# Optimization experiments

Hardware: AMD Instinct MI355X
Metric: run time of the kernel (lower is better)

Reference implementation:

```python
import jax, jax.numpy as jnp
import numpy as np

B, D, DC, K = 65536, 768, 192, 100  # batch patterns, hidden_dim, codebook_hidden, num_clusters
LN_EPS = 1e-5


def setup_inputs() -> dict:
    key = jax.random.key(0)
    ks = jax.random.split(key, 12)
    w = lambda k, shape: (jax.random.normal(k, shape, jnp.float32) * 0.02)
    return {
        "hidden": jax.random.normal(ks[0], (B, D), jnp.float32),
        "W_low": w(ks[1], (DC, D)),   # nn.Linear(hidden_dim, codebook_hidden), torch (out,in)
        "b_low": jnp.zeros((DC,), jnp.float32),
        "ln_g": jnp.ones((DC,), jnp.float32),
        "ln_b": jnp.zeros((DC,), jnp.float32),
        "Wq": w(ks[2], (DC, DC)),
        "Wk": w(ks[3], (DC, DC)),
        "Wv": w(ks[4], (DC, DC)),
        "Wo": w(ks[5], (DC, DC)),
        "codebook": w(ks[6], (K, DC)),  # vp_codebook.weight
        "W_high": w(ks[7], (D, DC)),    # nn.Linear(codebook_hidden, hidden_dim)
        "b_high": jnp.zeros((D,), jnp.float32),
    }


def reference(hidden, W_low, b_low, ln_g, ln_b, Wq, Wk, Wv, Wo, codebook, W_high, b_high):
    # low projection: 768 -> 192
    pat = hidden @ W_low.T + b_low  # [B, DC]
    # LayerNorm over last dim
    mu = jnp.mean(pat, axis=-1, keepdims=True)
    var = jnp.mean(jnp.square(pat - mu), axis=-1, keepdims=True)
    pat = (pat - mu) * jax.lax.rsqrt(var + LN_EPS) * ln_g + ln_b
    # CrossAttention against codebook with NEGATED scores (distance-like)
    q = pat @ Wq.T            # [B, DC]
    k = codebook @ Wk.T       # [K, DC]
    v = codebook @ Wv.T       # [K, DC]
    scores = -(q @ k.T)       # [B, K]
    attn_w = jax.nn.softmax(scores, axis=-1)
    attn_out = (attn_w @ v) @ Wo.T  # [B, DC]
    # argmin over attention weights -> codebook selection + gather
    idx = jnp.argmin(attn_w, axis=-1)   # [B] int
    z_q = codebook[idx]                 # [B, DC]
    # high projection on both branches
    pat_h = attn_out @ W_high.T + b_high  # [B, D]
    zq_h = z_q @ W_high.T + b_high        # [B, D]
    # straight-through estimator: pat + (z_q - pat).detach()
    return pat_h + jax.lax.stop_gradient(zq_h - pat_h)
```

## Files before the change

### kernel.cpp

```cpp
#include <hip/hip_runtime.h>

#define NB    65536
#define DIN   768
#define DCB   192
#define KCL   100
#define NJ    112
#define RT    128
#define KC    64

#define OFF_KTIL 0
#define OFF_S    19200
#define OFF_CS   38400
#define OFF_U    38512
#define OFF_T    38624
#define OFF_MT   38736
#define OFF_ZH   124752
#define OFF_FLAG 201552


__global__ void kA1(const float* __restrict__ cb, const float* __restrict__ Wk,
                    float* __restrict__ ktil, int* __restrict__ flag) {
  __shared__ float cbrow[DCB];
  int j = blockIdx.x, i = threadIdx.x;
  if (j == 0 && i == 0) *flag = 0;
  cbrow[i] = cb[j*DCB + i];
  __syncthreads();
  const float4* wr = (const float4*)&Wk[(size_t)i * DCB];
  double s0 = 0.0, s1 = 0.0;
  #pragma unroll 4
  for (int m4 = 0; m4 < DCB/4; m4++) {
    float4 w = wr[m4];
    s0 += (double)w.x * (double)cbrow[m4*4+0] + (double)w.z * (double)cbrow[m4*4+2];
    s1 += (double)w.y * (double)cbrow[m4*4+1] + (double)w.w * (double)cbrow[m4*4+3];
  }
  ktil[j*DCB+i] = (float)(s0 + s1);
}

__global__ void kA2(const float* __restrict__ Wq, const float* __restrict__ ktil,
                    const float* __restrict__ ln_g, const float* __restrict__ ln_b,
                    const float* __restrict__ b_low,
                    float* __restrict__ S, float* __restrict__ csum,
                    float* __restrict__ tv, float* __restrict__ u,
                    int* __restrict__ flag) {
  __shared__ float krow[DCB];
  __shared__ double red[DCB];
  int j = blockIdx.x, c = threadIdx.x;
  krow[c] = ktil[j*DCB + c];
  __syncthreads();
  double a0 = 0.0, a1 = 0.0;
  #pragma unroll 4
  for (int i = 0; i < DCB; i += 2) {
    a0 += (double)Wq[i*DCB+c]     * (double)krow[i];
    a1 += (double)Wq[(i+1)*DCB+c] * (double)krow[i+1];
  }
  double a = a0 + a1;
  float Sv = ln_g[c] * (float)a;
  S[j*DCB+c] = Sv;

  red[c] = (double)Sv; __syncthreads();
  if (c == 0) {
    double p0=0,p1=0,p2=0,p3=0;
    for (int i = 0; i < DCB; i += 4) { p0+=red[i]; p1+=red[i+1]; p2+=red[i+2]; p3+=red[i+3]; }
    csum[j] = (float)(p0+p1+p2+p3);
  }
  __syncthreads();
  red[c] = (double)ln_b[c] * a; __syncthreads();
  if (c == 0) {
    double p0=0,p1=0,p2=0,p3=0;
    for (int i = 0; i < DCB; i += 4) { p0+=red[i]; p1+=red[i+1]; p2+=red[i+2]; p3+=red[i+3]; }
    float tf = (float)(p0+p1+p2+p3); tv[j] = tf;
    if (tf != 0.0f) atomicOr(flag, 1);
  }
  __syncthreads();
  red[c] = (double)b_low[c] * (double)Sv; __syncthreads();
  if (c == 0) {
    double p0=0,p1=0,p2=0,p3=0;
    for (int i = 0; i < DCB; i += 4) { p0+=red[i]; p1+=red[i+1]; p2+=red[i+2]; p3+=red[i+3]; }
    u[j] = (float)(p0+p1+p2+p3);
  }
  __syncthreads();
  if (j == 0) {
    red[c] = (double)b_low[c]; __syncthreads();
    if (c == 0) {
      double p0=0,p1=0,p2=0,p3=0;
      for (int i = 0; i < DCB; i += 4) { p0+=red[i]; p1+=red[i+1]; p2+=red[i+2]; p3+=red[i+3]; }
      u[KCL] = (float)((p0+p1+p2+p3) / (double)DCB);
      for (int p = KCL+1; p < NJ; p++) u[p] = 0.f;
      for (int p = KCL;   p < NJ; p++) { csum[p] = 0.f; tv[p] = 0.f; }
    }
  }
}

__global__ void kA3(const float* __restrict__ W_low, const float* __restrict__ S,
                    float* __restrict__ Mt) {
  __shared__ float srow[DCB];
  int j = blockIdx.x, t = threadIdx.x;
  if (j < KCL && t < DCB) srow[t] = S[j*DCB + t];
  __syncthreads();
  if (j < KCL) {
    double a0 = 0.0, a1 = 0.0, a2 = 0.0;
    for (int c = 0; c < DCB; c++) {
      float sc = srow[c];
      a0 += (double)W_low[(size_t)c*DIN + t]       * (double)sc;
      a1 += (double)W_low[(size_t)c*DIN + t + 256] * (double)sc;
      a2 += (double)W_low[(size_t)c*DIN + t + 512] * (double)sc;
    }
    Mt[(size_t)j*DIN + t]       = (float)a0;
    Mt[(size_t)j*DIN + t + 256] = (float)a1;
    Mt[(size_t)j*DIN + t + 512] = (float)a2;
  } else if (j == KCL) {
    double a0 = 0.0, a1 = 0.0, a2 = 0.0;
    for (int c = 0; c < DCB; c++) {
      a0 += (double)W_low[(size_t)c*DIN + t];
      a1 += (double)W_low[(size_t)c*DIN + t + 256];
      a2 += (double)W_low[(size_t)c*DIN + t + 512];
    }
    Mt[(size_t)j*DIN + t]       = (float)(a0 / (double)DCB);
    Mt[(size_t)j*DIN + t + 256] = (float)(a1 / (double)DCB);
    Mt[(size_t)j*DIN + t + 512] = (float)(a2 / (double)DCB);
  } else {
    Mt[(size_t)j*DIN + t]       = 0.f;
    Mt[(size_t)j*DIN + t + 256] = 0.f;
    Mt[(size_t)j*DIN + t + 512] = 0.f;
  }
}

__global__ void kA4(const float* __restrict__ cb, const float* __restrict__ W_high,
                    const float* __restrict__ b_high, float* __restrict__ ZH) {
  __shared__ float cbrow[DCB];
  int j = blockIdx.x, t = threadIdx.x;
  if (t < DCB) cbrow[t] = cb[j*DCB + t];
  __syncthreads();
  #pragma unroll
  for (int kd = 0; kd < 3; kd++) {
    int d = t + 256*kd;
    const float4* wr = (const float4*)&W_high[(size_t)d * DCB];
    double s0 = 0.0, s1 = 0.0;
    #pragma unroll 4
    for (int c4 = 0; c4 < DCB/4; c4++) {
      float4 w = wr[c4];
      s0 += (double)w.x * (double)cbrow[c4*4+0] + (double)w.z * (double)cbrow[c4*4+2];
      s1 += (double)w.y * (double)cbrow[c4*4+1] + (double)w.w * (double)cbrow[c4*4+3];
    }
    ZH[(size_t)j*DIN + d] = (float)(s0 + s1 + (double)b_high[d]);
  }
}

__global__ __launch_bounds__(256, 2)
void kB(const float* __restrict__ hidden, float* __restrict__ out,
        const float* __restrict__ Mt, const float* __restrict__ u,
        const float* __restrict__ csum, const float* __restrict__ ZH,
        const int* __restrict__ flag,
        const float* __restrict__ S, const float* __restrict__ tv,
        const float* __restrict__ W_low, const float* __restrict__ b_low) {
  __shared__ float hs[RT * 68];
  __shared__ float Ms[NJ * 68];
  __shared__ float uc[NJ];
  __shared__ float cs[NJ];
  __shared__ int   idxs[RT];
  const int tid = threadIdx.x;
  const int r0  = blockIdx.x * RT;

  if (*flag == 0) {
    const int jg = tid & 15, rg = tid >> 4;
    const int jbase = jg * 7, rbase = rg * 8;
    const int lane = tid & 63;
    const int grpbase = lane & ~15;
    if (tid < NJ) { uc[tid] = u[tid]; cs[tid] = csum[tid]; }

    float acc[8][7];
    #pragma unroll
    for (int i = 0; i < 8; i++)
      #pragma unroll
      for (int j = 0; j < 7; j++) acc[i][j] = 0.f;

    for (int ck = 0; ck < DIN / KC; ck++) {
      const int k0 = ck * KC;
      __syncthreads();
      #pragma unroll
      for (int i = 0; i < 8; i++) {
        int f = tid + 256 * i;
        int r = f >> 4, k4 = f & 15;
        float4 v = *(const float4*)&hidden[(size_t)(r0 + r) * DIN + k0 + k4 * 4];
        *(float4*)&hs[r * 68 + k4 * 4] = v;
      }
      #pragma unroll
      for (int i = 0; i < 7; i++) {
        int f = tid + 256 * i;
        int j = f >> 4, k4 = f & 15;
        float4 v = *(const float4*)&Mt[(size_t)j * DIN + k0 + k4 * 4];
        *(float4*)&Ms[j * 68 + k4 * 4] = v;
      }
      __syncthreads();
      #pragma unroll 4
      for (int kk = 0; kk < KC; kk += 4) {
        float4 h4[8], m4[7];
        #pragma unroll
        for (int j = 0; j < 7; j++) m4[j] = *(const float4*)&Ms[(jbase + j) * 68 + kk];
        #pragma unroll
        for (int i = 0; i < 8; i++) h4[i] = *(const float4*)&hs[(rbase + i) * 68 + kk];
        #pragma unroll
        for (int i = 0; i < 8; i++)
          #pragma unroll
          for (int j = 0; j < 7; j++) {
            acc[i][j] += h4[i].x * m4[j].x;
            acc[i][j] += h4[i].y * m4[j].y;
            acc[i][j] += h4[i].z * m4[j].z;
            acc[i][j] += h4[i].w * m4[j].w;
          }
      }
    }
    const float u100 = uc[KCL];
    #pragma unroll
    for (int i = 0; i < 8; i++) {
      float mu = __shfl(acc[i][2], grpbase + 14, 64) + u100;
      float lb = -3.4e38f; int li = 0;
      #pragma unroll
      for (int j = 0; j < 7; j++) {
        int jj = jbase + j;
        float s = acc[i][j] + uc[jj] - mu * cs[jj];
        s = (jj < KCL) ? s : -3.4e38f;
        if (s > lb) { lb = s; li = jj; }
      }
      #pragma unroll
      for (int off = 1; off < 16; off <<= 1) {
        float ov = __shfl_xor(lb, off, 64);
        int   oi = __shfl_xor(li, off, 64);
        if (ov > lb || (ov == lb && oi < li)) { lb = ov; li = oi; }
      }
      if (jg == 0) idxs[rbase + i] = li;
    }
    __syncthreads();
    for (int i = 0; i < 96; i++) {
      int f = tid + 256 * i;
      int r = f / 192, d4 = f - r * 192;
      int idx = idxs[r];
      float4 v = *(const float4*)&ZH[(size_t)idx * DIN + d4 * 4];
      *(float4*)&out[(size_t)(r0 + r) * DIN + d4 * 4] = v;
    }
  } else {
    float* hrow = hs;
    float* patv = hs + 768;
    float* redf = hs + 960;
    float* Gsc  = Ms;
    for (int rr = 0; rr < RT; rr++) {
      const size_t row = (size_t)(r0 + rr);
      __syncthreads();
      for (int d = tid; d < DIN; d += 256) hrow[d] = hidden[row * DIN + d];
      __syncthreads();
      if (tid < DCB) {
        float a = b_low[tid];
        for (int d = 0; d < DIN; d++) a += hrow[d] * W_low[(size_t)tid * DIN + d];
        patv[tid] = a;
      }
      __syncthreads();
      if (tid == 0) {
        float mu = 0.f; for (int c = 0; c < DCB; c++) mu += patv[c]; mu /= (float)DCB;
        float var = 0.f; for (int c = 0; c < DCB; c++) { float dd = patv[c] - mu; var += dd * dd; }
        var /= (float)DCB;
        redf[0] = mu; redf[1] = rsqrtf(var + 1e-5f);
      }
      __syncthreads();
      if (tid < DCB) patv[tid] = (patv[tid] - redf[0]) * redf[1];
      __syncthreads();
      if (tid < KCL) {
        float s = tv[tid];
        for (int c = 0; c < DCB; c++) s += patv[c] * S[(size_t)tid * DCB + c];
        Gsc[tid] = s;
      }
      __syncthreads();
      if (tid == 0) {
        float best = -3.4e38f; int bi = 0;
        for (int j = 0; j < KCL; j++) if (Gsc[j] > best) { best = Gsc[j]; bi = j; }
        idxs[0] = bi;
      }
      __syncthreads();
      {
        int idx = idxs[0];
        for (int d4 = tid; d4 < DIN / 4; d4 += 256) {
          float4 v = *(const float4*)&ZH[(size_t)idx * DIN + d4 * 4];
          *(float4*)&out[row * DIN + d4 * 4] = v;
        }
      }
    }
  }
}

extern "C" void kernel_launch(void* const* d_in, const int* in_sizes, int n_in,
                              void* d_out, int out_size, void* d_ws, size_t ws_size,
                              hipStream_t stream) {
  const float* hidden = (const float*)d_in[0];
  const float* W_low  = (const float*)d_in[1];
  const float* b_low  = (const float*)d_in[2];
  const float* ln_g   = (const float*)d_in[3];
  const float* ln_b   = (const float*)d_in[4];
  const float* Wq     = (const float*)d_in[5];
  const float* Wk     = (const float*)d_in[6];
  const float* cb     = (const float*)d_in[9];
  const float* W_high = (const float*)d_in[10];
  const float* b_high = (const float*)d_in[11];
  float* out = (float*)d_out;
  float* ws  = (float*)d_ws;

  float* ktil = ws + OFF_KTIL;
  float* S    = ws + OFF_S;
  float* csum = ws + OFF_CS;
  float* u    = ws + OFF_U;
  float* tv   = ws + OFF_T;
  float* Mt   = ws + OFF_MT;
  float* ZH   = ws + OFF_ZH;
  int*   flag = (int*)(ws + OFF_FLAG);

  kA1<<<KCL, DCB, 0, stream>>>(cb, Wk, ktil, flag);
  kA2<<<KCL, DCB, 0, stream>>>(Wq, ktil, ln_g, ln_b, b_low, S, csum, tv, u, flag);
  kA3<<<NJ,  256, 0, stream>>>(W_low, S, Mt);
  kA4<<<KCL, 256, 0, stream>>>(cb, W_high, b_high, ZH);
  kB<<<NB / RT, 256, 0, stream>>>(hidden, out, Mt, u, csum, ZH, flag,
                                  S, tv, W_low, b_low);
}
```

Before: 538.7 us.

## Use fp16 MFMA for score GEMM with fp64 recheck of near-tie rows

```diff
diff --git a/kernel.cpp b/kernel.cpp
--- a/kernel.cpp
+++ b/kernel.cpp
@@ -5,24 +5,32 @@
 #define DCB   192
 #define KCL   100
 #define NJ    112
-#define RT    128
-#define KC    64
-
-#define OFF_KTIL 0
-#define OFF_S    19200
-#define OFF_CS   38400
-#define OFF_U    38512
-#define OFF_T    38624
-#define OFF_MT   38736
-#define OFF_ZH   124752
-#define OFF_FLAG 201552
+
+#define OFF_S    0
+#define OFF_CS   19200
+#define OFF_U    19312
+#define OFF_T    19424
+#define OFF_ZH   19536
+#define OFF_FLAG 96336
+#define OFF_CNT  96337
+#define OFF_MTH  96340
+#define OFF_KTIL 96340
+#define OFF_LIST 139348
+
+#define MARGIN 1e-4f
+#define MTSC   64.0f
+#define SCINV  0.015625f
+
+typedef __attribute__((ext_vector_type(8))) _Float16 half8;
+typedef __attribute__((ext_vector_type(4))) float    f32x4;
 
 
 __global__ void kA1(const float* __restrict__ cb, const float* __restrict__ Wk,
-                    float* __restrict__ ktil, int* __restrict__ flag) {
+                    float* __restrict__ ktil, int* __restrict__ flag,
+                    int* __restrict__ cnt) {
   __shared__ float cbrow[DCB];
   int j = blockIdx.x, i = threadIdx.x;
-  if (j == 0 && i == 0) *flag = 0;
+  if (j == 0 && i == 0) { *flag = 0; *cnt = 0; }
   cbrow[i] = cb[j*DCB + i];
   __syncthreads();
   const float4* wr = (const float4*)&Wk[(size_t)i * DCB];
@@ -92,11 +100,12 @@
 }
 
 __global__ void kA3(const float* __restrict__ W_low, const float* __restrict__ S,
-                    float* __restrict__ Mt) {
+                    _Float16* __restrict__ Mth) {
   __shared__ float srow[DCB];
   int j = blockIdx.x, t = threadIdx.x;
   if (j < KCL && t < DCB) srow[t] = S[j*DCB + t];
   __syncthreads();
+  float v0, v1, v2;
   if (j < KCL) {
     double a0 = 0.0, a1 = 0.0, a2 = 0.0;
     for (int c = 0; c < DCB; c++) {
@@ -105,9 +114,7 @@
       a1 += (double)W_low[(size_t)c*DIN + t + 256] * (double)sc;
       a2 += (double)W_low[(size_t)c*DIN + t + 512] * (double)sc;
     }
-    Mt[(size_t)j*DIN + t]       = (float)a0;
-    Mt[(size_t)j*DIN + t + 256] = (float)a1;
-    Mt[(size_t)j*DIN + t + 512] = (float)a2;
+    v0 = (float)a0; v1 = (float)a1; v2 = (float)a2;
   } else if (j == KCL) {
     double a0 = 0.0, a1 = 0.0, a2 = 0.0;
     for (int c = 0; c < DCB; c++) {
@@ -115,14 +122,15 @@
       a1 += (double)W_low[(size_t)c*DIN + t + 256];
       a2 += (double)W_low[(size_t)c*DIN + t + 512];
     }
-    Mt[(size_t)j*DIN + t]       = (float)(a0 / (double)DCB);
-    Mt[(size_t)j*DIN + t + 256] = (float)(a1 / (double)DCB);
-    Mt[(size_t)j*DIN + t + 512] = (float)(a2 / (double)DCB);
+    v0 = (float)(a0 / (double)DCB);
+    v1 = (float)(a1 / (double)DCB);
+    v2 = (float)(a2 / (double)DCB);
   } else {
-    Mt[(size_t)j*DIN + t]       = 0.f;
-    Mt[(size_t)j*DIN + t + 256] = 0.f;
-    Mt[(size_t)j*DIN + t + 512] = 0.f;
-  }
+    v0 = v1 = v2 = 0.f;
+  }
+  Mth[(size_t)j*DIN + t]       = (_Float16)(v0 * MTSC);
+  Mth[(size_t)j*DIN + t + 256] = (_Float16)(v1 * MTSC);
+  Mth[(size_t)j*DIN + t + 512] = (_Float16)(v2 * MTSC);
 }
 
 __global__ void kA4(const float* __restrict__ cb, const float* __restrict__ W_high,
@@ -146,111 +154,120 @@
   }
 }
 
-__global__ __launch_bounds__(256, 2)
+__global__ __launch_bounds__(256, 3)
 void kB(const float* __restrict__ hidden, float* __restrict__ out,
-        const float* __restrict__ Mt, const float* __restrict__ u,
+        const _Float16* __restrict__ Mth, const float* __restrict__ u,
         const float* __restrict__ csum, const float* __restrict__ ZH,
-        const int* __restrict__ flag,
+        const int* __restrict__ flag, int* __restrict__ cnt,
+        unsigned short* __restrict__ list,
         const float* __restrict__ S, const float* __restrict__ tv,
         const float* __restrict__ W_low, const float* __restrict__ b_low) {
-  __shared__ float hs[RT * 68];
-  __shared__ float Ms[NJ * 68];
-  __shared__ float uc[NJ];
-  __shared__ float cs[NJ];
-  __shared__ int   idxs[RT];
   const int tid = threadIdx.x;
-  const int r0  = blockIdx.x * RT;
-
   if (*flag == 0) {
-    const int jg = tid & 15, rg = tid >> 4;
-    const int jbase = jg * 7, rbase = rg * 8;
     const int lane = tid & 63;
-    const int grpbase = lane & ~15;
-    if (tid < NJ) { uc[tid] = u[tid]; cs[tid] = csum[tid]; }
-
-    float acc[8][7];
-    #pragma unroll
-    for (int i = 0; i < 8; i++)
+    const int wv   = tid >> 6;
+    const int lj   = lane & 15, lk = lane >> 4;
+    const int R    = blockIdx.x * 64 + wv * 16;
+
+    const float*    Ap = hidden + (size_t)(R + lj) * DIN + lk * 8;
+    const _Float16* Bp = Mth    + (size_t)lj       * DIN + lk * 8;
+
+    f32x4 acc[7];
+    #pragma unroll
+    for (int nj = 0; nj < 7; nj++) acc[nj] = (f32x4){0.f, 0.f, 0.f, 0.f};
+
+    float4 a0 = *(const float4*)(Ap);
+    float4 a1 = *(const float4*)(Ap + 4);
+    half8 b[7];
+    #pragma unroll
+    for (int nj = 0; nj < 7; nj++) b[nj] = *(const half8*)(Bp + nj * 16 * DIN);
+
+    #pragma unroll
+    for (int t = 0; t < 24; t++) {
+      float4 na0, na1; half8 nb[7];
+      if (t < 23) {
+        const float* Ap2 = Ap + (t + 1) * 32;
+        na0 = *(const float4*)(Ap2);
+        na1 = *(const float4*)(Ap2 + 4);
+        const _Float16* Bp2 = Bp + (t + 1) * 32;
+        #pragma unroll
+        for (int nj = 0; nj < 7; nj++) nb[nj] = *(const half8*)(Bp2 + nj * 16 * DIN);
+      }
+      half8 ah;
+      ah[0] = (_Float16)a0.x; ah[1] = (_Float16)a0.y;
+      ah[2] = (_Float16)a0.z; ah[3] = (_Float16)a0.w;
+      ah[4] = (_Float16)a1.x; ah[5] = (_Float16)a1.y;
+      ah[6] = (_Float16)a1.z; ah[7] = (_Float16)a1.w;
       #pragma unroll
-      for (int j = 0; j < 7; j++) acc[i][j] = 0.f;
-
-    for (int ck = 0; ck < DIN / KC; ck++) {
-      const int k0 = ck * KC;
-      __syncthreads();
+      for (int nj = 0; nj < 7; nj++)
+        acc[nj] = __builtin_amdgcn_mfma_f32_16x16x32_f16(ah, b[nj], acc[nj], 0, 0, 0);
+      if (t < 23) {
+        a0 = na0; a1 = na1;
+        #pragma unroll
+        for (int nj = 0; nj < 7; nj++) b[nj] = nb[nj];
+      }
+    }
+
+    float uj[7], cj[7];
+    #pragma unroll
+    for (int nj = 0; nj < 7; nj++) { int j = nj*16 + lj; uj[nj] = u[j]; cj[nj] = csum[j]; }
+    const float u100 = u[KCL];
+
+    int idxr[4];
+    #pragma unroll
+    for (int r = 0; r < 4; r++) {
+      float mu = __shfl(acc[6][r], (lane & 48) + 4, 64) * SCINV + u100;
+      float b1 = -3.4e38f, b2 = -3.4e38f; int i1 = 0;
       #pragma unroll
-      for (int i = 0; i < 8; i++) {
-        int f = tid + 256 * i;
-        int r = f >> 4, k4 = f & 15;
-        float4 v = *(const float4*)&hidden[(size_t)(r0 + r) * DIN + k0 + k4 * 4];
-        *(float4*)&hs[r * 68 + k4 * 4] = v;
-      }
-      #pragma unroll
-      for (int i = 0; i < 7; i++) {
-        int f = tid + 256 * i;
-        int j = f >> 4, k4 = f & 15;
-        float4 v = *(const float4*)&Mt[(size_t)j * DIN + k0 + k4 * 4];
-        *(float4*)&Ms[j * 68 + k4 * 4] = v;
-      }
-      __syncthreads();
-      #pragma unroll 4
-      for (int kk = 0; kk < KC; kk += 4) {
-        float4 h4[8], m4[7];
-        #pragma unroll
-        for (int j = 0; j < 7; j++) m4[j] = *(const float4*)&Ms[(jbase + j) * 68 + kk];
-        #pragma unroll
-        for (int i = 0; i < 8; i++) h4[i] = *(const float4*)&hs[(rbase + i) * 68 + kk];
-        #pragma unroll
-        for (int i = 0; i < 8; i++)
-          #pragma unroll
-          for (int j = 0; j < 7; j++) {
-            acc[i][j] += h4[i].x * m4[j].x;
-            acc[i][j] += h4[i].y * m4[j].y;
-            acc[i][j] += h4[i].z * m4[j].z;
-            acc[i][j] += h4[i].w * m4[j].w;
-          }
-      }
-    }
-    const float u100 = uc[KCL];
-    #pragma unroll
-    for (int i = 0; i < 8; i++) {
-      float mu = __shfl(acc[i][2], grpbase + 14, 64) + u100;
-      float lb = -3.4e38f; int li = 0;
-      #pragma unroll
-      for (int j = 0; j < 7; j++) {
-        int jj = jbase + j;
-        float s = acc[i][j] + uc[jj] - mu * cs[jj];
-        s = (jj < KCL) ? s : -3.4e38f;
-        if (s > lb) { lb = s; li = jj; }
+      for (int nj = 0; nj < 7; nj++) {
+        int j = nj*16 + lj;
+        float s = acc[nj][r] * SCINV + uj[nj] - mu * cj[nj];
+        s = (j < KCL) ? s : -3.4e38f;
+        if (s > b1) { b2 = b1; b1 = s; i1 = j; }
+        else if (s > b2) { b2 = s; }
       }
       #pragma unroll
       for (int off = 1; off < 16; off <<= 1) {
-        float ov = __shfl_xor(lb, off, 64);
-        int   oi = __shfl_xor(li, off, 64);
-        if (ov > lb || (ov == lb && oi < li)) { lb = ov; li = oi; }
-      }
-      if (jg == 0) idxs[rbase + i] = li;
-    }
-    __syncthreads();
-    for (int i = 0; i < 96; i++) {
-      int f = tid + 256 * i;
-      int r = f / 192, d4 = f - r * 192;
-      int idx = idxs[r];
-      float4 v = *(const float4*)&ZH[(size_t)idx * DIN + d4 * 4];
-      *(float4*)&out[(size_t)(r0 + r) * DIN + d4 * 4] = v;
+        float ob1 = __shfl_xor(b1, off, 64);
+        int   oi1 = __shfl_xor(i1, off, 64);
+        float ob2 = __shfl_xor(b2, off, 64);
+        if (ob1 > b1 || (ob1 == b1 && oi1 < i1)) {
+          b2 = fmaxf(b1, fmaxf(b2, ob2)); b1 = ob1; i1 = oi1;
+        } else {
+          b2 = fmaxf(ob1, fmaxf(b2, ob2));
+        }
+      }
+      idxr[r] = i1;
+      if (lj == 0 && (b1 - b2) <= MARGIN) {
+        int p = atomicAdd(cnt, 1);
+        list[p] = (unsigned short)(R + lk * 4 + r);
+      }
+    }
+
+    #pragma unroll
+    for (int m = 0; m < 16; m++) {
+      int idx = __shfl(idxr[m & 3], (m >> 2) << 4, 64);
+      const float4* zs = (const float4*)(ZH + (size_t)idx * DIN);
+      float4* od = (float4*)(out + (size_t)(R + m) * DIN);
+      od[lane]       = zs[lane];
+      od[lane + 64]  = zs[lane + 64];
+      od[lane + 128] = zs[lane + 128];
     }
   } else {
-    float* hrow = hs;
-    float* patv = hs + 768;
-    float* redf = hs + 960;
-    float* Gsc  = Ms;
-    for (int rr = 0; rr < RT; rr++) {
+    __shared__ float hrow2[DIN];
+    __shared__ float patv[DCB];
+    __shared__ float redf[2];
+    __shared__ float Gsc[KCL];
+    __shared__ int   sidx;
+    const int r0 = blockIdx.x * 64;
+    for (int rr = 0; rr < 64; rr++) {
       const size_t row = (size_t)(r0 + rr);
       __syncthreads();
-      for (int d = tid; d < DIN; d += 256) hrow[d] = hidden[row * DIN + d];
+      for (int d = tid; d < DIN; d += 256) hrow2[d] = hidden[row * DIN + d];
       __syncthreads();
       if (tid < DCB) {
         float a = b_low[tid];
-        for (int d = 0; d < DIN; d++) a += hrow[d] * W_low[(size_t)tid * DIN + d];
+        for (int d = 0; d < DIN; d++) a += hrow2[d] * W_low[(size_t)tid * DIN + d];
         patv[tid] = a;
       }
       __syncthreads();
@@ -272,15 +289,74 @@
       if (tid == 0) {
         float best = -3.4e38f; int bi = 0;
         for (int j = 0; j < KCL; j++) if (Gsc[j] > best) { best = Gsc[j]; bi = j; }
-        idxs[0] = bi;
+        sidx = bi;
       }
       __syncthreads();
       {
-        int idx = idxs[0];
+        int idx = sidx;
         for (int d4 = tid; d4 < DIN / 4; d4 += 256) {
           float4 v = *(const float4*)&ZH[(size_t)idx * DIN + d4 * 4];
           *(float4*)&out[row * DIN + d4 * 4] = v;
         }
+      }
+    }
+  }
+}
+
+__global__ void kC(const float* __restrict__ hidden, float* __restrict__ out,
+                   const float* __restrict__ W_low, const float* __restrict__ b_low,
+                   const float* __restrict__ S, const float* __restrict__ ZH,
+                   const int* __restrict__ cnt, const unsigned short* __restrict__ list) {
+  __shared__ float  hrow[DIN];
+  __shared__ double pat[DCB];
+  __shared__ double smu;
+  __shared__ double sc[KCL];
+  __shared__ int    bidx;
+  const int n = *cnt;
+  const int tid = threadIdx.x;
+  for (int it = blockIdx.x; it < n; it += gridDim.x) {
+    const int row = (int)list[it];
+    __syncthreads();
+    for (int d = tid; d < DIN; d += 256) hrow[d] = hidden[(size_t)row * DIN + d];
+    __syncthreads();
+    if (tid < DCB) {
+      const float* wl = W_low + (size_t)tid * DIN;
+      double a = (double)b_low[tid];
+      for (int d = 0; d < DIN; d += 4) {
+        a += (double)hrow[d]   * (double)wl[d]
+           + (double)hrow[d+1] * (double)wl[d+1]
+           + (double)hrow[d+2] * (double)wl[d+2]
+           + (double)hrow[d+3] * (double)wl[d+3];
+      }
+      pat[tid] = a;
+    }
+    __syncthreads();
+    if (tid == 0) {
+      double m = 0.0;
+      for (int c = 0; c < DCB; c++) m += pat[c];
+      smu = m / (double)DCB;
+    }
+    __syncthreads();
+    if (tid < KCL) {
+      const float* sr = S + (size_t)tid * DCB;
+      const double mu = smu;
+      double a = 0.0;
+      for (int c = 0; c < DCB; c++) a += (pat[c] - mu) * (double)sr[c];
+      sc[tid] = a;
+    }
+    __syncthreads();
+    if (tid == 0) {
+      double best = -1e300; int bi = 0;
+      for (int j = 0; j < KCL; j++)
+        if (sc[j] > best) { best = sc[j]; bi = j; }
+      bidx = bi;
+    }
+    __syncthreads();
+    {
+      const int idx = bidx;
+      for (int d4 = tid; d4 < DIN / 4; d4 += 256) {
+        float4 v = *(const float4*)(ZH + (size_t)idx * DIN + d4 * 4);
+        *(float4*)(out + (size_t)row * DIN + d4 * 4) = v;
       }
     }
   }
@@ -302,19 +378,22 @@
   float* out = (float*)d_out;
   float* ws  = (float*)d_ws;
 
-  float* ktil = ws + OFF_KTIL;
-  float* S    = ws + OFF_S;
-  float* csum = ws + OFF_CS;
-  float* u    = ws + OFF_U;
-  float* tv   = ws + OFF_T;
-  float* Mt   = ws + OFF_MT;
-  float* ZH   = ws + OFF_ZH;
-  int*   flag = (int*)(ws + OFF_FLAG);
-
-  kA1<<<KCL, DCB, 0, stream>>>(cb, Wk, ktil, flag);
+  float*          S    = ws + OFF_S;
+  float*          csum = ws + OFF_CS;
+  float*          u    = ws + OFF_U;
+  float*          tv   = ws + OFF_T;
+  float*          ZH   = ws + OFF_ZH;
+  int*            flag = (int*)(ws + OFF_FLAG);
+  int*            cnt  = (int*)(ws + OFF_CNT);
+  _Float16*       Mth  = (_Float16*)(ws + OFF_MTH);
+  float*          ktil = ws + OFF_KTIL;
+  unsigned short* list = (unsigned short*)(ws + OFF_LIST);
+
+  kA1<<<KCL, DCB, 0, stream>>>(cb, Wk, ktil, flag, cnt);
   kA2<<<KCL, DCB, 0, stream>>>(Wq, ktil, ln_g, ln_b, b_low, S, csum, tv, u, flag);
-  kA3<<<NJ,  256, 0, stream>>>(W_low, S, Mt);
+  kA3<<<NJ,  256, 0, stream>>>(W_low, S, Mth);
   kA4<<<KCL, 256, 0, stream>>>(cb, W_high, b_high, ZH);
-  kB<<<NB / RT, 256, 0, stream>>>(hidden, out, Mt, u, csum, ZH, flag,
+  kB<<<NB / 64, 256, 0, stream>>>(hidden, out, Mth, u, csum, ZH, flag, cnt, list,
                                   S, tv, W_low, b_low);
-}
+  kC<<<2048, 256, 0, stream>>>(hidden, out, W_low, b_low, S, ZH, cnt, list);
+}
```

Result: slower. 633.8 us (+17.6%).
